# Kernel optimization log

Measured on AMD Instinct MI355X. Metric: run time of the kernel, lower is better.

Reference implementation:

```python
import jax, jax.numpy as jnp
import numpy as np

B, S, D = 8, 4096, 256
NUM_WINDOW = 8
WIN = S // NUM_WINDOW          # 512
H = 2                          # num_heads
K = D                          # key_dim = d_model per source
DFF = 1024
LN_EPS = 1e-3                  # keras LayerNormalization default epsilon


def _layer_norm(x, g, b):
    mu = jnp.mean(x, axis=-1, keepdims=True)
    var = jnp.mean(jnp.square(x - mu), axis=-1, keepdims=True)
    return (x - mu) * jax.lax.rsqrt(var + LN_EPS) * g + b


def setup_inputs() -> dict:
    key = jax.random.key(0)
    ks = jax.random.split(key, 12)
    s = 0.02
    inp = {
        "x": jax.random.normal(ks[0], (B, S, D), dtype=jnp.float32),
        # MHA projections (keras MultiHeadAttention layout)
        "Wq": jax.random.normal(ks[1], (D, H, K), dtype=jnp.float32) * s,
        "bq": jnp.zeros((H, K), dtype=jnp.float32),
        "Wk": jax.random.normal(ks[2], (D, H, K), dtype=jnp.float32) * s,
        "bk": jnp.zeros((H, K), dtype=jnp.float32),
        "Wv": jax.random.normal(ks[3], (D, H, K), dtype=jnp.float32) * s,
        "bv": jnp.zeros((H, K), dtype=jnp.float32),
        "Wo": jax.random.normal(ks[4], (H, K, D), dtype=jnp.float32) * s,
        "bo": jnp.zeros((D,), dtype=jnp.float32),
        "ln1_g": jnp.ones((D,), dtype=jnp.float32),
        "ln1_b": jnp.zeros((D,), dtype=jnp.float32),
        # FeedForward
        "W1": jax.random.normal(ks[5], (D, DFF), dtype=jnp.float32) * s,
        "b1": jnp.zeros((DFF,), dtype=jnp.float32),
        "W2": jax.random.normal(ks[6], (DFF, D), dtype=jnp.float32) * s,
        "b2": jnp.zeros((D,), dtype=jnp.float32),
        "ln2_g": jnp.ones((D,), dtype=jnp.float32),
        "ln2_b": jnp.zeros((D,), dtype=jnp.float32),
    }
    return inp


def reference(x, Wq, bq, Wk, bk, Wv, bv, Wo, bo, ln1_g, ln1_b,
              W1, b1, W2, b2, ln2_g, ln2_b):
    # --- Localized self-attention: block-diagonal over NUM_WINDOW windows ---
    xw = x.reshape(B, NUM_WINDOW, WIN, D)               # [b, w, s, d]
    q = jnp.einsum('bwsd,dhk->bwshk', xw, Wq) + bq      # [b, w, s, h, k]
    k = jnp.einsum('bwsd,dhk->bwshk', xw, Wk) + bk
    v = jnp.einsum('bwsd,dhk->bwshk', xw, Wv) + bv
    scores = jnp.einsum('bwshk,bwthk->bwhst', q, k) / jnp.sqrt(
        jnp.asarray(K, dtype=x.dtype))                  # [b, w, h, s, t]
    attn = jax.nn.softmax(scores, axis=-1)
    ctx = jnp.einsum('bwhst,bwthk->bwshk', attn, v)     # [b, w, s, h, k]
    attn_out = jnp.einsum('bwshk,hkd->bwsd', ctx, Wo) + bo
    attn_out = attn_out.reshape(B, S, D)                # concat over windows
    x = _layer_norm(x + attn_out, ln1_g, ln1_b)
    # --- FeedForward (dropout inactive at inference) ---
    h = jax.nn.relu(x @ W1 + b1)
    ff = h @ W2 + b2
    return _layer_norm(x + ff, ln2_g, ln2_b)
```

## Files before the change

### kernel.cpp

```cpp
#include <hip/hip_runtime.h>

typedef unsigned short u16;
typedef short short8 __attribute__((ext_vector_type(8)));
typedef float f32x4 __attribute__((ext_vector_type(4)));

#define AS1C const __attribute__((address_space(1))) void*
#define AS3P __attribute__((address_space(3))) void*

__device__ __forceinline__ u16 f2b(float f) {
  unsigned u = __float_as_uint(f);
  return (u16)((u + 0x7fffu + ((u >> 16) & 1u)) >> 16);
}
__device__ __forceinline__ float b2f(u16 h) {
  return __uint_as_float((unsigned)h << 16);
}

#define BB 8
#define SS 4096
#define DD 256
#define MTOK (BB*SS)

#define OFF_WQKVT  ((size_t)0)
#define OFF_WOT    ((size_t)786432)
#define OFF_W1T    ((size_t)1048576)
#define OFF_W2T    ((size_t)1572864)
#define OFF_BQKV   ((size_t)2097152)
#define OFF_XB     ((size_t)2103296)
#define OFF_QKV    ((size_t)18880512)
#define OFF_YB     ((size_t)52434944)
#define OFF_HB     ((size_t)69212160)
#define OFF_VT     ((size_t)119543808)
#define OFF_CTX    ((size_t)153098240)

__global__ __launch_bounds__(256) void cast_x_kernel(const float* __restrict__ x,
                                                     u16* __restrict__ xb) {
  size_t i = ((size_t)blockIdx.x * 256 + threadIdx.x) * 4;
  float4 v = *(const float4*)(x + i);
  ushort4 o;
  o.x = f2b(v.x); o.y = f2b(v.y); o.z = f2b(v.z); o.w = f2b(v.w);
  *(ushort4*)(xb + i) = o;
}

__global__ __launch_bounds__(256) void prep_w_kernel(
    const float* __restrict__ Wq, const float* __restrict__ Wk, const float* __restrict__ Wv,
    const float* __restrict__ Wo, const float* __restrict__ W1, const float* __restrict__ W2,
    const float* __restrict__ bq, const float* __restrict__ bk, const float* __restrict__ bv,
    u16* __restrict__ wqkvt, u16* __restrict__ wot, u16* __restrict__ w1t,
    u16* __restrict__ w2t, float* __restrict__ bqkv)
{
  for (int i = blockIdx.x * 256 + threadIdx.x; i < 1050112; i += 1024 * 256) {
    if (i < 393216) {
      int n = i >> 8, d = i & 255;
      const float* W = (n < 512) ? Wq : (n < 1024) ? Wk : Wv;
      int nn = n & 511;
      wqkvt[i] = f2b(W[d * 512 + nn]);
    } else if (i < 524288) {
      int j = i - 393216;
      int dout = j >> 9, hk = j & 511;
      wot[j] = f2b(Wo[hk * 256 + dout]);
    } else if (i < 786432) {
      int j = i - 524288;
      int f = j >> 8, d = j & 255;
      w1t[j] = f2b(W1[d * 1024 + f]);
    } else if (i < 1048576) {
      int j = i - 786432;
      int d = j >> 10, f = j & 1023;
      w2t[j] = f2b(W2[f * 256 + d]);
    } else {
      int n = i - 1048576;
      bqkv[n] = (n < 512) ? bq[n] : (n < 1024) ? bk[n - 512] : bv[n - 1024];
    }
  }
}

__global__ __launch_bounds__(256) void gemm_nres(
    const u16* __restrict__ A, const u16* __restrict__ BT,
    const float* __restrict__ bias, u16* __restrict__ C,
    u16* __restrict__ vt, int N, int vbase, int relu)
{
  __shared__ __align__(16) u16 lds[16384];
  const int tid = threadIdx.x, lane = tid & 63, wid = tid >> 6;
  const int ln = lane & 15, quad = lane >> 4;
  const int pn = blockIdx.x >> 5;
  const int mg = blockIdx.x & 31;
  const int wno = (wid >> 1) << 5;
  const int wmo = (wid & 1) << 4;
  const long mbase = (long)mg << 10;
  const int nb = pn << 6;
  const u16* Bp = BT + (size_t)nb * 256;
  const u16* Ap = A + (size_t)mbase * 256;

#pragma unroll
  for (int p = 0; p < 8; p++) {
    const int s = p * 256 + tid;
    const int row = s >> 5, pc = s & 31;
    const int c = pc ^ (row & 31);
    __builtin_amdgcn_global_load_lds(
        (AS1C)(Bp + (size_t)row * 256 + c * 8), (AS3P)(lds + s * 8), 16, 0, 0);
  }
  __syncthreads();
  short8 breg[2][8];
#pragma unroll
  for (int j = 0; j < 2; j++) {
    const int row = wno + j * 16 + ln;
#pragma unroll
    for (int ks = 0; ks < 8; ks++)
      breg[j][ks] = *(const short8*)(lds + row * 256 + (((ks << 2) + quad) ^ (row & 31)) * 8);
  }
  __syncthreads();

#pragma unroll
  for (int p = 0; p < 4; p++) {
    const int s = p * 256 + tid;
    const int row = s >> 5, pc = s & 31;
    const int c = pc ^ (row & 31);
    __builtin_amdgcn_global_load_lds(
        (AS1C)(Ap + (size_t)row * 256 + c * 8), (AS3P)(lds + s * 8), 16, 0, 0);
  }

  for (int it = 0; it < 32; it++) {
    const int cur = it & 1;
    const u16* Ab = lds + cur * 8192;
    __syncthreads();
    if (it + 1 < 32) {
      const u16* An = Ap + (size_t)(it + 1) * 32 * 256;
      u16* Ax = lds + (cur ^ 1) * 8192;
#pragma unroll
      for (int p = 0; p < 4; p++) {
        const int s = p * 256 + tid;
        const int row = s >> 5, pc = s & 31;
        const int c = pc ^ (row & 31);
        __builtin_amdgcn_global_load_lds(
            (AS1C)(An + (size_t)row * 256 + c * 8), (AS3P)(Ax + s * 8), 16, 0, 0);
      }
    }
    f32x4 acc[2];
    acc[0] = (f32x4){0.f, 0.f, 0.f, 0.f};
    acc[1] = (f32x4){0.f, 0.f, 0.f, 0.f};
    const int r0 = wmo + ln;
#pragma unroll
    for (int ks = 0; ks < 8; ks++) {
      const short8 a0 = *(const short8*)(Ab + r0 * 256 + (((ks << 2) + quad) ^ (r0 & 31)) * 8);
      acc[0] = __builtin_amdgcn_mfma_f32_16x16x32_bf16(breg[0][ks], a0, acc[0], 0, 0, 0);
      acc[1] = __builtin_amdgcn_mfma_f32_16x16x32_bf16(breg[1][ks], a0, acc[1], 0, 0, 0);
    }
    const long m = mbase + it * 32 + wmo + ln;
    if (nb < vbase) {
#pragma unroll
      for (int j = 0; j < 2; j++) {
        const int n0 = nb + wno + j * 16 + quad * 4;
        f32x4 v = acc[j];
        const float4 b4 = *(const float4*)(bias + n0);
        v[0] += b4.x; v[1] += b4.y; v[2] += b4.z; v[3] += b4.w;
        if (relu) {
#pragma unroll
          for (int r = 0; r < 4; r++) v[r] = fmaxf(v[r], 0.f);
        }
        ushort4 ob;
        ob.x = f2b(v[0]); ob.y = f2b(v[1]); ob.z = f2b(v[2]); ob.w = f2b(v[3]);
        *(ushort4*)(C + (size_t)m * N + n0) = ob;
      }
    } else {
      const int bw = (int)(m >> 9), t = (int)(m & 511);
#pragma unroll
      for (int j = 0; j < 2; j++) {
        const int n0 = nb + wno + j * 16 + quad * 4;
        const int rel = n0 - vbase;
        const int h = rel >> 8, k0 = rel & 255;
        u16* vp = vt + (size_t)(bw * 2 + h) * 131072 + (size_t)k0 * 512 + t;
        const float4 b4 = *(const float4*)(bias + n0);
        vp[0]    = f2b(acc[j][0] + b4.x);
        vp[512]  = f2b(acc[j][1] + b4.y);
        vp[1024] = f2b(acc[j][2] + b4.z);
        vp[1536] = f2b(acc[j][3] + b4.w);
      }
    }
  }
}

__global__ __launch_bounds__(512, 4) void attn_fused(const u16* __restrict__ qkv,
                                                     const u16* __restrict__ vt,
                                                     u16* __restrict__ ctx)
{
  __shared__ __align__(16) u16 lds[38912];
  const int tid = threadIdx.x, lane = tid & 63, wid = tid >> 6;
  const int ln = lane & 15, quad = lane >> 4;
  const int bat = blockIdx.x & 127, mt = blockIdx.x >> 7;
  const int bw = bat >> 1, h = bat & 1;
  const u16* Qb = qkv + (size_t)bw * 786432 + (size_t)h * 256 + (size_t)(mt * 64) * 1536;
  const u16* Kb = qkv + (size_t)bw * 786432 + 512 + (size_t)h * 256;
  const u16* Vb = vt + (size_t)bat * 131072;
  const int wn = wid * 64;
  float* red1 = (float*)(lds + 36864);
  float* red2 = red1 + 512;

  f32x4 acc[4][4];
#pragma unroll
  for (int i = 0; i < 4; i++)
#pragma unroll
    for (int j = 0; j < 4; j++) acc[i][j] = (f32x4){0.f, 0.f, 0.f, 0.f};

  if (tid < 256) {
    const int row = tid >> 2, c = tid & 3;
    __builtin_amdgcn_global_load_lds(
        (AS1C)(Qb + (size_t)row * 1536 + c * 8), (AS3P)(lds + tid * 8), 16, 0, 0);
  }
#pragma unroll
  for (int p = 0; p < 4; p++) {
    const int s = p * 512 + tid;
    const int row = s >> 2, c = s & 3;
    __builtin_amdgcn_global_load_lds(
        (AS1C)(Kb + (size_t)row * 1536 + c * 8), (AS3P)(lds + 4096 + s * 8), 16, 0, 0);
  }

  for (int ki = 0; ki < 8; ki++) {
    const int cur = ki & 1;
    __syncthreads();
    if (ki < 7) {
      const int kt = (ki + 1) * 32, nxt = cur ^ 1;
      if (tid < 256) {
        const int row = tid >> 2, c = tid & 3;
        __builtin_amdgcn_global_load_lds(
            (AS1C)(Qb + (size_t)row * 1536 + kt + c * 8),
            (AS3P)(lds + nxt * 2048 + tid * 8), 16, 0, 0);
      }
#pragma unroll
      for (int p = 0; p < 4; p++) {
        const int s = p * 512 + tid;
        const int row = s >> 2, c = s & 3;
        __builtin_amdgcn_global_load_lds(
            (AS1C)(Kb + (size_t)row * 1536 + kt + c * 8),
            (AS3P)(lds + 4096 + nxt * 16384 + s * 8), 16, 0, 0);
      }
    }
    short8 a[4], b[4];
#pragma unroll
    for (int i = 0; i < 4; i++)
      a[i] = *(const short8*)(lds + cur * 2048 + (i * 16 + ln) * 32 + quad * 8);
#pragma unroll
    for (int j = 0; j < 4; j++)
      b[j] = *(const short8*)(lds + 4096 + cur * 16384 + (wn + j * 16 + ln) * 32 + quad * 8);
    __builtin_amdgcn_s_setprio(1);
#pragma unroll
    for (int i = 0; i < 4; i++)
#pragma unroll
      for (int j = 0; j < 4; j++)
        acc[i][j] = __builtin_amdgcn_mfma_f32_16x16x32_bf16(b[j], a[i], acc[i][j], 0, 0, 0);
    __builtin_amdgcn_s_setprio(0);
  }

  float rowmax[4], rowsum[4];
#pragma unroll
  for (int i = 0; i < 4; i++) {
    float m = -1e30f;
#pragma unroll
    for (int j = 0; j < 4; j++)
#pragma unroll
      for (int r = 0; r < 4; r++) m = fmaxf(m, acc[i][j][r]);
    m = fmaxf(m, __shfl_xor(m, 16));
    m = fmaxf(m, __shfl_xor(m, 32));
    if (quad == 0) red1[wid * 64 + i * 16 + ln] = m;
  }
  __syncthreads();

#pragma unroll
  for (int p = 0; p < 4; p++) {
    const int s = p * 512 + tid;
    const int row = s >> 3, pc = s & 7;
    const int cc = pc ^ (row & 7);
    __builtin_amdgcn_global_load_lds(
        (AS1C)(Vb + (size_t)row * 512 + cc * 8), (AS3P)(lds + s * 8), 16, 0, 0);
  }

#pragma unroll
  for (int i = 0; i < 4; i++) {
    float m = -1e30f;
#pragma unroll
    for (int w = 0; w < 8; w++) m = fmaxf(m, red1[w * 64 + i * 16 + ln]);
    rowmax[i] = m;
  }
#pragma unroll
  for (int i = 0; i < 4; i++) {
    float s = 0.f;
#pragma unroll
    for (int j = 0; j < 4; j++)
#pragma unroll
      for (int r = 0; r < 4; r++) {
        const float e = __expf((acc[i][j][r] - rowmax[i]) * 0.0625f);
        acc[i][j][r] = e; s += e;
      }
    s += __shfl_xor(s, 16);
    s += __shfl_xor(s, 32);
    if (quad == 0) red2[wid * 64 + i * 16 + ln] = s;
  }
  __syncthreads();
#pragma unroll
  for (int i = 0; i < 4; i++) {
    float s = 0.f;
#pragma unroll
    for (int w = 0; w < 8; w++) s += red2[w * 64 + i * 16 + ln];
    rowsum[i] = 1.f / s;
  }

  ushort4 pb[4][4];
#pragma unroll
  for (int i = 0; i < 4; i++)
#pragma unroll
    for (int j = 0; j < 4; j++) {
      pb[i][j].x = f2b(acc[i][j][0] * rowsum[i]);
      pb[i][j].y = f2b(acc[i][j][1] * rowsum[i]);
      pb[i][j].z = f2b(acc[i][j][2] * rowsum[i]);
      pb[i][j].w = f2b(acc[i][j][3] * rowsum[i]);
    }

  u16* Pb = lds + 32768;
  const int wno = wid * 32;
  f32x4 o[4][2];
#pragma unroll
  for (int i = 0; i < 4; i++) {
    o[i][0] = (f32x4){0.f, 0.f, 0.f, 0.f};
    o[i][1] = (f32x4){0.f, 0.f, 0.f, 0.f};
  }

  for (int c = 0; c < 8; c++) {
    __syncthreads();
    if (wid == c) {
#pragma unroll
      for (int i = 0; i < 4; i++)
#pragma unroll
        for (int j = 0; j < 4; j++)
          *(ushort4*)(Pb + (i * 16 + ln) * 72 + j * 16 + quad * 4) = pb[i][j];
    }
    __syncthreads();
    if (c < 7) {
      const int nb = (c + 1) & 1;
#pragma unroll
      for (int p = 0; p < 4; p++) {
        const int s = p * 512 + tid;
        const int row = s >> 3, pc = s & 7;
        const int cc = pc ^ (row & 7);
        __builtin_amdgcn_global_load_lds(
            (AS1C)(Vb + (size_t)row * 512 + (c + 1) * 64 + cc * 8),
            (AS3P)(lds + nb * 16384 + s * 8), 16, 0, 0);
      }
    }
    const u16* Vc = lds + (c & 1) * 16384;
    __builtin_amdgcn_s_setprio(1);
#pragma unroll
    for (int ks = 0; ks < 2; ks++) {
      short8 ap[4];
#pragma unroll
      for (int i = 0; i < 4; i++)
        ap[i] = *(const short8*)(Pb + (i * 16 + ln) * 72 + ks * 32 + quad * 8);
#pragma unroll
      for (int j = 0; j < 2; j++) {
        const int kV = wno + j * 16 + ln;
        const short8 bv = *(const short8*)(Vc + kV * 64 + (((ks << 2) + quad) ^ (kV & 7)) * 8);
#pragma unroll
        for (int i = 0; i < 4; i++)
          o[i][j] = __builtin_amdgcn_mfma_f32_16x16x32_bf16(bv, ap[i], o[i][j], 0, 0, 0);
      }
    }
    __builtin_amdgcn_s_setprio(0);
  }

  const size_t tokr0 = (size_t)bw * 512 + mt * 64;
#pragma unroll
  for (int i = 0; i < 4; i++) {
    const size_t row = tokr0 + i * 16 + ln;
#pragma unroll
    for (int j = 0; j < 2; j++) {
      const int col = h * 256 + wno + j * 16 + quad * 4;
      ushort4 ob;
      ob.x = f2b(o[i][j][0]); ob.y = f2b(o[i][j][1]);
      ob.z = f2b(o[i][j][2]); ob.w = f2b(o[i][j][3]);
      *(ushort4*)(ctx + row * 512 + col) = ob;
    }
  }
}

__global__ __launch_bounds__(256) void gemm_ln(
    const u16* __restrict__ A, const u16* __restrict__ BT,
    const float* __restrict__ bias, const u16* __restrict__ residb,
    const float* __restrict__ g, const float* __restrict__ beta,
    float* __restrict__ yout, u16* __restrict__ ybout, int K)
{
  __shared__ __align__(16) u16 As[64 * 32];
  __shared__ __align__(16) u16 Bs[256 * 32];
  __shared__ float redS[4][64], redQ[4][64];
  const int tid = threadIdx.x, lane = tid & 63, wid = tid >> 6;
  const int ln = lane & 15, quad = lane >> 4;
  const long bm = (long)blockIdx.x * 64;
  const int wn = wid * 64;
  const u16* Ab = A + (size_t)bm * K;

  f32x4 acc[4][4];
#pragma unroll
  for (int i = 0; i < 4; i++)
#pragma unroll
    for (int j = 0; j < 4; j++) acc[i][j] = (f32x4){0.f, 0.f, 0.f, 0.f};

  for (int kt = 0; kt < K; kt += 32) {
    {
      const int row = tid >> 2, c = tid & 3;
      __builtin_amdgcn_global_load_lds(
          (AS1C)(Ab + (size_t)row * K + kt + c * 8), (AS3P)(As + tid * 8), 16, 0, 0);
    }
#pragma unroll
    for (int p = 0; p < 4; p++) {
      const int s = p * 256 + tid;
      const int row = s >> 2, c = s & 3;
      __builtin_amdgcn_global_load_lds(
          (AS1C)(BT + (size_t)row * K + kt + c * 8), (AS3P)(Bs + s * 8), 16, 0, 0);
    }
    __syncthreads();
    short8 a[4], b[4];
#pragma unroll
    for (int i = 0; i < 4; i++) a[i] = *(const short8*)(As + (i * 16 + ln) * 32 + quad * 8);
#pragma unroll
    for (int j = 0; j < 4; j++) b[j] = *(const short8*)(Bs + (wn + j * 16 + ln) * 32 + quad * 8);
#pragma unroll
    for (int i = 0; i < 4; i++)
#pragma unroll
      for (int j = 0; j < 4; j++)
        acc[i][j] = __builtin_amdgcn_mfma_f32_16x16x32_bf16(b[j], a[i], acc[i][j], 0, 0, 0);
    __syncthreads();
  }

#pragma unroll
  for (int i = 0; i < 4; i++) {
    const long gm = bm + i * 16 + ln;
    float s = 0.f, q = 0.f;
#pragma unroll
    for (int j = 0; j < 4; j++) {
      const int n0 = wn + j * 16 + quad * 4;
      const float4 b4 = *(const float4*)(bias + n0);
      const ushort4 r4 = *(const ushort4*)(residb + (size_t)gm * 256 + n0);
      acc[i][j][0] += b4.x + b2f(r4.x);
      acc[i][j][1] += b4.y + b2f(r4.y);
      acc[i][j][2] += b4.z + b2f(r4.z);
      acc[i][j][3] += b4.w + b2f(r4.w);
#pragma unroll
      for (int r = 0; r < 4; r++) { s += acc[i][j][r]; q += acc[i][j][r] * acc[i][j][r]; }
    }
    s += __shfl_xor(s, 16); s += __shfl_xor(s, 32);
    q += __shfl_xor(q, 16); q += __shfl_xor(q, 32);
    if (quad == 0) { redS[wid][i * 16 + ln] = s; redQ[wid][i * 16 + ln] = q; }
  }
  __syncthreads();
#pragma unroll
  for (int i = 0; i < 4; i++) {
    const long gm = bm + i * 16 + ln;
    float s = 0.f, q = 0.f;
#pragma unroll
    for (int w = 0; w < 4; w++) { s += redS[w][i * 16 + ln]; q += redQ[w][i * 16 + ln]; }
    const float mu = s * (1.f / 256.f);
    const float inv = rsqrtf(q * (1.f / 256.f) - mu * mu + 1e-3f);
#pragma unroll
    for (int j = 0; j < 4; j++) {
      const int n0 = wn + j * 16 + quad * 4;
      const float4 gg = *(const float4*)(g + n0);
      const float4 bb = *(const float4*)(beta + n0);
      float o0 = (acc[i][j][0] - mu) * inv * gg.x + bb.x;
      float o1 = (acc[i][j][1] - mu) * inv * gg.y + bb.y;
      float o2 = (acc[i][j][2] - mu) * inv * gg.z + bb.z;
      float o3 = (acc[i][j][3] - mu) * inv * gg.w + bb.w;
      const size_t off = (size_t)gm * 256 + n0;
      if (yout) {
        float4 o4; o4.x = o0; o4.y = o1; o4.z = o2; o4.w = o3;
        *(float4*)(yout + off) = o4;
      }
      if (ybout) {
        ushort4 ob;
        ob.x = f2b(o0); ob.y = f2b(o1); ob.z = f2b(o2); ob.w = f2b(o3);
        *(ushort4*)(ybout + off) = ob;
      }
    }
  }
}

extern "C" void kernel_launch(void* const* d_in, const int* in_sizes, int n_in,
                              void* d_out, int out_size, void* d_ws, size_t ws_size,
                              hipStream_t stream) {
  (void)in_sizes; (void)n_in; (void)out_size; (void)ws_size;
  const float* x    = (const float*)d_in[0];
  const float* Wq   = (const float*)d_in[1];
  const float* bq   = (const float*)d_in[2];
  const float* Wk   = (const float*)d_in[3];
  const float* bk   = (const float*)d_in[4];
  const float* Wv   = (const float*)d_in[5];
  const float* bv   = (const float*)d_in[6];
  const float* Wo   = (const float*)d_in[7];
  const float* bo   = (const float*)d_in[8];
  const float* ln1g = (const float*)d_in[9];
  const float* ln1b = (const float*)d_in[10];
  const float* W1   = (const float*)d_in[11];
  const float* b1   = (const float*)d_in[12];
  const float* W2   = (const float*)d_in[13];
  const float* b2   = (const float*)d_in[14];
  const float* ln2g = (const float*)d_in[15];
  const float* ln2b = (const float*)d_in[16];
  float* out = (float*)d_out;

  char* ws = (char*)d_ws;
  u16*   WQKVT = (u16*)(ws + OFF_WQKVT);
  u16*   WOT   = (u16*)(ws + OFF_WOT);
  u16*   W1T   = (u16*)(ws + OFF_W1T);
  u16*   W2T   = (u16*)(ws + OFF_W2T);
  float* BQKV  = (float*)(ws + OFF_BQKV);
  u16*   XB    = (u16*)(ws + OFF_XB);
  u16*   QKV   = (u16*)(ws + OFF_QKV);
  u16*   YB    = (u16*)(ws + OFF_YB);
  u16*   HB    = (u16*)(ws + OFF_HB);
  u16*   VT    = (u16*)(ws + OFF_VT);
  u16*   CTX   = (u16*)(ws + OFF_CTX);

  cast_x_kernel<<<8192, 256, 0, stream>>>(x, XB);
  prep_w_kernel<<<1024, 256, 0, stream>>>(Wq, Wk, Wv, Wo, W1, W2, bq, bk, bv,
                                          WQKVT, WOT, W1T, W2T, BQKV);
  gemm_nres<<<768, 256, 0, stream>>>(XB, WQKVT, BQKV, QKV, VT, 1536, 1024, 0);
  attn_fused<<<1024, 512, 0, stream>>>(QKV, VT, CTX);
  gemm_ln<<<512, 256, 0, stream>>>(CTX, WOT, bo, XB, ln1g, ln1b, nullptr, YB, 512);
  gemm_nres<<<512, 256, 0, stream>>>(YB, W1T, b1, HB, nullptr, 1024, 1 << 30, 1);
  gemm_ln<<<512, 256, 0, stream>>>(HB, W2T, b2, YB, ln2g, ln2b, out, nullptr, 1024);
}
```

Baseline: 338.0 us.

## Swizzle LDS layout in attention and double-buffer gemm_ln K loop

Applies an XOR swizzle to the 16-byte chunk index when staging Q/K tiles into LDS in the attention kernel and A/B tiles in gemm_ln, with the same swizzle on fragment reads, to reduce LDS bank conflicts. gemm_ln also moves from a single-buffer load/sync/compute/sync loop to a double-buffered prefetch with one barrier per iteration, and raises MFMA priority around the inner product. This doubles gemm_ln's LDS footprint, which may reduce occupancy.

```diff
diff --git a/kernel.cpp b/kernel.cpp
--- a/kernel.cpp
+++ b/kernel.cpp
@@ -191,6 +191,7 @@
   const u16* Kb = qkv + (size_t)bw * 786432 + 512 + (size_t)h * 256;
   const u16* Vb = vt + (size_t)bat * 131072;
   const int wn = wid * 64;
+  const int qsw = (ln >> 1) & 3;
   float* red1 = (float*)(lds + 36864);
   float* red2 = red1 + 512;
 
@@ -201,14 +202,16 @@
     for (int j = 0; j < 4; j++) acc[i][j] = (f32x4){0.f, 0.f, 0.f, 0.f};
 
   if (tid < 256) {
-    const int row = tid >> 2, c = tid & 3;
+    const int row = tid >> 2;
+    const int c = (tid & 3) ^ ((row >> 1) & 3);
     __builtin_amdgcn_global_load_lds(
         (AS1C)(Qb + (size_t)row * 1536 + c * 8), (AS3P)(lds + tid * 8), 16, 0, 0);
   }
 #pragma unroll
   for (int p = 0; p < 4; p++) {
     const int s = p * 512 + tid;
-    const int row = s >> 2, c = s & 3;
+    const int row = s >> 2;
+    const int c = (s & 3) ^ ((row >> 1) & 3);
     __builtin_amdgcn_global_load_lds(
         (AS1C)(Kb + (size_t)row * 1536 + c * 8), (AS3P)(lds + 4096 + s * 8), 16, 0, 0);
   }
@@ -219,7 +222,8 @@
     if (ki < 7) {
       const int kt = (ki + 1) * 32, nxt = cur ^ 1;
       if (tid < 256) {
-        const int row = tid >> 2, c = tid & 3;
+        const int row = tid >> 2;
+        const int c = (tid & 3) ^ ((row >> 1) & 3);
         __builtin_amdgcn_global_load_lds(
             (AS1C)(Qb + (size_t)row * 1536 + kt + c * 8),
             (AS3P)(lds + nxt * 2048 + tid * 8), 16, 0, 0);
@@ -227,7 +231,8 @@
 #pragma unroll
       for (int p = 0; p < 4; p++) {
         const int s = p * 512 + tid;
-        const int row = s >> 2, c = s & 3;
+        const int row = s >> 2;
+        const int c = (s & 3) ^ ((row >> 1) & 3);
         __builtin_amdgcn_global_load_lds(
             (AS1C)(Kb + (size_t)row * 1536 + kt + c * 8),
             (AS3P)(lds + 4096 + nxt * 16384 + s * 8), 16, 0, 0);
@@ -236,10 +241,10 @@
     short8 a[4], b[4];
 #pragma unroll
     for (int i = 0; i < 4; i++)
-      a[i] = *(const short8*)(lds + cur * 2048 + (i * 16 + ln) * 32 + quad * 8);
+      a[i] = *(const short8*)(lds + cur * 2048 + ((i * 16 + ln) * 4 + (quad ^ qsw)) * 8);
 #pragma unroll
     for (int j = 0; j < 4; j++)
-      b[j] = *(const short8*)(lds + 4096 + cur * 16384 + (wn + j * 16 + ln) * 32 + quad * 8);
+      b[j] = *(const short8*)(lds + 4096 + cur * 16384 + ((wn + j * 16 + ln) * 4 + (quad ^ qsw)) * 8);
     __builtin_amdgcn_s_setprio(1);
 #pragma unroll
     for (int i = 0; i < 4; i++)
@@ -385,14 +390,16 @@
     const float* __restrict__ g, const float* __restrict__ beta,
     float* __restrict__ yout, u16* __restrict__ ybout, int K)
 {
-  __shared__ __align__(16) u16 As[64 * 32];
-  __shared__ __align__(16) u16 Bs[256 * 32];
+  __shared__ __align__(16) u16 As[2][2048];
+  __shared__ __align__(16) u16 Bs[2][8192];
   __shared__ float redS[4][64], redQ[4][64];
   const int tid = threadIdx.x, lane = tid & 63, wid = tid >> 6;
   const int ln = lane & 15, quad = lane >> 4;
+  const int qsw = (ln >> 1) & 3;
   const long bm = (long)blockIdx.x * 64;
   const int wn = wid * 64;
   const u16* Ab = A + (size_t)bm * K;
+  const int nk = K >> 5;
 
   f32x4 acc[4][4];
 #pragma unroll
@@ -400,31 +407,53 @@
 #pragma unroll
     for (int j = 0; j < 4; j++) acc[i][j] = (f32x4){0.f, 0.f, 0.f, 0.f};
 
-  for (int kt = 0; kt < K; kt += 32) {
-    {
-      const int row = tid >> 2, c = tid & 3;
-      __builtin_amdgcn_global_load_lds(
-          (AS1C)(Ab + (size_t)row * K + kt + c * 8), (AS3P)(As + tid * 8), 16, 0, 0);
-    }
+  {
+    const int row = tid >> 2;
+    const int c = (tid & 3) ^ ((row >> 1) & 3);
+    __builtin_amdgcn_global_load_lds(
+        (AS1C)(Ab + (size_t)row * K + c * 8), (AS3P)(&As[0][0] + tid * 8), 16, 0, 0);
 #pragma unroll
     for (int p = 0; p < 4; p++) {
       const int s = p * 256 + tid;
-      const int row = s >> 2, c = s & 3;
+      const int br = s >> 2;
+      const int bc = (s & 3) ^ ((br >> 1) & 3);
       __builtin_amdgcn_global_load_lds(
-          (AS1C)(BT + (size_t)row * K + kt + c * 8), (AS3P)(Bs + s * 8), 16, 0, 0);
-    }
+          (AS1C)(BT + (size_t)br * K + bc * 8), (AS3P)(&Bs[0][0] + s * 8), 16, 0, 0);
+    }
+  }
+
+  for (int kti = 0; kti < nk; kti++) {
+    const int cur = kti & 1;
     __syncthreads();
+    if (kti + 1 < nk) {
+      const int kt = (kti + 1) * 32, nxt = cur ^ 1;
+      const int row = tid >> 2;
+      const int c = (tid & 3) ^ ((row >> 1) & 3);
+      __builtin_amdgcn_global_load_lds(
+          (AS1C)(Ab + (size_t)row * K + kt + c * 8), (AS3P)(&As[nxt][0] + tid * 8), 16, 0, 0);
+#pragma unroll
+      for (int p = 0; p < 4; p++) {
+        const int s = p * 256 + tid;
+        const int br = s >> 2;
+        const int bc = (s & 3) ^ ((br >> 1) & 3);
+        __builtin_amdgcn_global_load_lds(
+            (AS1C)(BT + (size_t)br * K + kt + bc * 8), (AS3P)(&Bs[nxt][0] + s * 8), 16, 0, 0);
+      }
+    }
     short8 a[4], b[4];
 #pragma unroll
-    for (int i = 0; i < 4; i++) a[i] = *(const short8*)(As + (i * 16 + ln) * 32 + quad * 8);
-#pragma unroll
-    for (int j = 0; j < 4; j++) b[j] = *(const short8*)(Bs + (wn + j * 16 + ln) * 32 + quad * 8);
+    for (int i = 0; i < 4; i++)
+      a[i] = *(const short8*)(&As[cur][0] + ((i * 16 + ln) * 4 + (quad ^ qsw)) * 8);
+#pragma unroll
+    for (int j = 0; j < 4; j++)
+      b[j] = *(const short8*)(&Bs[cur][0] + ((wn + j * 16 + ln) * 4 + (quad ^ qsw)) * 8);
+    __builtin_amdgcn_s_setprio(1);
 #pragma unroll
     for (int i = 0; i < 4; i++)
 #pragma unroll
       for (int j = 0; j < 4; j++)
         acc[i][j] = __builtin_amdgcn_mfma_f32_16x16x32_bf16(b[j], a[i], acc[i][j], 0, 0, 0);
-    __syncthreads();
+    __builtin_amdgcn_s_setprio(0);
   }
 
 #pragma unroll
```

New measurement: 333.4 us. Within noise of the previous version (-1.4%).
